# Kernel tuning notes

Measured on AMD Instinct MI355X. Metric: run time of the kernel, lower is better.

Reference implementation:

```python
import jax, jax.numpy as jnp
import numpy as np

DIM = 256
HEADS = 4
HEAD_DIM = DIM // HEADS          # 64
KEY_DIM = HEAD_DIM // 2          # 32 (attn_ratio=0.5)
HIDDEN = DIM + 2 * KEY_DIM * HEADS  # 512
B, H, W = 2, 64, 64
EPS = 1e-5


def _conv2d(x, w, groups=1, pad=0):
    return jax.lax.conv_general_dilated(
        x, w, window_strides=(1, 1), padding=[(pad, pad), (pad, pad)],
        dimension_numbers=('NCHW', 'OIHW', 'NCHW'), feature_group_count=groups)


def _bn(x, g, b, m, v):
    scale = g / jnp.sqrt(v + EPS)
    return x * scale[None, :, None, None] + (b - m * scale)[None, :, None, None]


def setup_inputs() -> dict:
    key = jax.random.key(0)
    ks = jax.random.split(key, 16)
    d = {
        'x': jax.random.normal(ks[0], (B, DIM, H, W), jnp.float32),
        'qkv_w': jax.random.normal(ks[1], (HIDDEN, DIM, 1, 1), jnp.float32) * 0.05,
        'qkv_g': jax.random.uniform(ks[2], (HIDDEN,), jnp.float32, 0.5, 1.5),
        'qkv_b': jax.random.normal(ks[3], (HIDDEN,), jnp.float32) * 0.1,
        'qkv_m': jax.random.normal(ks[4], (HIDDEN,), jnp.float32) * 0.1,
        'qkv_v': jax.random.uniform(ks[5], (HIDDEN,), jnp.float32, 0.5, 1.5),
        'proj_w': jax.random.normal(ks[6], (DIM, DIM, 1, 1), jnp.float32) * 0.05,
        'proj_g': jax.random.uniform(ks[7], (DIM,), jnp.float32, 0.5, 1.5),
        'proj_b': jax.random.normal(ks[8], (DIM,), jnp.float32) * 0.1,
        'proj_m': jax.random.normal(ks[9], (DIM,), jnp.float32) * 0.1,
        'proj_v': jax.random.uniform(ks[10], (DIM,), jnp.float32, 0.5, 1.5),
        'pe_w': jax.random.normal(ks[11], (DIM, 1, 3, 3), jnp.float32) * 0.1,
        'pe_g': jax.random.uniform(ks[12], (DIM,), jnp.float32, 0.5, 1.5),
        'pe_b': jax.random.normal(ks[13], (DIM,), jnp.float32) * 0.1,
        'pe_m': jax.random.normal(ks[14], (DIM,), jnp.float32) * 0.1,
        'pe_v': jax.random.uniform(ks[15], (DIM,), jnp.float32, 0.5, 1.5),
    }
    return d


def reference(x, qkv_w, qkv_g, qkv_b, qkv_m, qkv_v,
              proj_w, proj_g, proj_b, proj_m, proj_v,
              pe_w, pe_g, pe_b, pe_m, pe_v):
    b, c, h, w = x.shape
    n = h * w
    scale = KEY_DIM ** -0.5

    qkv = _bn(_conv2d(x, qkv_w), qkv_g, qkv_b, qkv_m, qkv_v)  # [b, hidden, h, w]
    qkv = qkv.reshape(b, HEADS, 2 * KEY_DIM + HEAD_DIM, n)
    q = qkv[:, :, :KEY_DIM]                       # [b, heads, key_dim, n]
    k = qkv[:, :, KEY_DIM:2 * KEY_DIM]            # [b, heads, key_dim, n]
    v = qkv[:, :, 2 * KEY_DIM:]                   # [b, heads, head_dim, n]

    # attn[b,h,i,j] = sum_d q[b,h,d,i] * k[b,h,d,j] * scale; softmax over j
    attn = jnp.einsum('bhdi,bhdj->bhij', q, k) * scale
    attn = jax.nn.softmax(attn, axis=-1)

    # y = v @ attn^T : out[b,h,d,i] = sum_j v[b,h,d,j] * attn[b,h,i,j]
    y = jnp.einsum('bhdj,bhij->bhdi', v, attn).reshape(b, c, h, w)

    pe = _bn(_conv2d(v.reshape(b, c, h, w), pe_w, groups=c, pad=1),
             pe_g, pe_b, pe_m, pe_v)
    y = y + pe
    return _bn(_conv2d(y, proj_w), proj_g, proj_b, proj_m, proj_v)
```

## Files before the change

kernel.cpp:

```cpp
#include <hip/hip_runtime.h>
#include <hip/hip_bf16.h>

#define NSP 4096
#define BEPS 1e-5f
#define JSPLIT 4
#define JCHUNK (NSP / JSPLIT)

using short8  = __attribute__((ext_vector_type(8))) short;
using f32x4   = __attribute__((ext_vector_type(4))) float;

#define SCALE_LOG2E 0.25500526940103816f

__device__ __forceinline__ float b2f(unsigned short u) {
  return __uint_as_float(((unsigned)u) << 16);
}
__device__ __forceinline__ float b2f_lo(unsigned w) {
  return __uint_as_float(w << 16);
}
__device__ __forceinline__ float b2f_hi(unsigned w) {
  return __uint_as_float(w & 0xffff0000u);
}
__device__ __forceinline__ unsigned short f2b(float x) {
  unsigned u = __float_as_uint(x);
  u += 0x7fffu + ((u >> 16) & 1u);
  return (unsigned short)(u >> 16);
}
__device__ __forceinline__ unsigned pk_bf16(float a, float b) {
  return ((unsigned)f2b(b) << 16) | (unsigned)f2b(a);
}
__device__ __forceinline__ unsigned pk2u(float a, float b) {
  __hip_bfloat162 h = __float22bfloat162_rn(float2{a, b});
  unsigned r;
  __builtin_memcpy(&r, &h, sizeof(r));
  return r;
}

__global__ __launch_bounds__(256) void cast_w_kernel(
    const float* __restrict__ qkv_w, const float* __restrict__ proj_w,
    unsigned short* __restrict__ wqb, unsigned short* __restrict__ wpb)
{
  const int i = blockIdx.x * 256 + threadIdx.x;
  if (i < 131072)       wqb[i] = f2b(qkv_w[i]);
  else                  wpb[i - 131072] = f2b(proj_w[i - 131072]);
}

__global__ __launch_bounds__(256) void transpose_x_kernel(
    const float* __restrict__ x, unsigned short* __restrict__ xT)
{
  const int n0 = blockIdx.x * 64, c0 = blockIdx.y * 64, b = blockIdx.z;
  __shared__ __align__(16) unsigned short tx[64][72];
  const int t = threadIdx.x;
  const int row = t >> 2;
  const int seg = t & 3;
  {
    const float* xp = x + ((size_t)(b * 256 + c0 + row)) * NSP + n0 + seg * 16;
    #pragma unroll
    for (int q4 = 0; q4 < 4; ++q4) {
      const float4 a = *reinterpret_cast<const float4*>(xp + q4 * 4);
      tx[seg * 16 + q4 * 4 + 0][row] = f2b(a.x);
      tx[seg * 16 + q4 * 4 + 1][row] = f2b(a.y);
      tx[seg * 16 + q4 * 4 + 2][row] = f2b(a.z);
      tx[seg * 16 + q4 * 4 + 3][row] = f2b(a.w);
    }
  }
  __syncthreads();
  const int nrow = t >> 2, ch = t & 3;
  unsigned short* op = xT + ((size_t)(b * NSP + n0 + nrow)) * 256 + c0 + ch * 16;
  *reinterpret_cast<float4*>(op)     = *reinterpret_cast<const float4*>(&tx[nrow][ch * 16]);
  *reinterpret_cast<float4*>(op + 8) = *reinterpret_cast<const float4*>(&tx[nrow][ch * 16 + 8]);
}

__global__ __launch_bounds__(256) void qkv_gemm_kernel(
    const unsigned short* __restrict__ xT, const unsigned short* __restrict__ wqb,
    const float* __restrict__ gg, const float* __restrict__ bb,
    const float* __restrict__ mm, const float* __restrict__ vv,
    unsigned short* __restrict__ qb, unsigned short* __restrict__ kb,
    unsigned short* __restrict__ vb)
{
  const int n0 = blockIdx.x * 128;
  const int cotile = blockIdx.y;
  const int b = blockIdx.z;
  const int co0 = cotile * 64;
  const int t = threadIdx.x;
  __shared__ __align__(16) unsigned short wt[64][136];
  __shared__ __align__(16) unsigned short xt[128][136];
  const int lane = t & 63, wave = t >> 6;
  const int m16 = lane & 15, quad = lane >> 4;

  f32x4 acc[8] = {};
  for (int kc = 0; kc < 2; ++kc) {
    if (kc) __syncthreads();
    {
      const unsigned short* wp = wqb + (size_t)(co0 + (t >> 2)) * 256 + kc * 128 + (t & 3) * 32;
      #pragma unroll
      for (int u = 0; u < 4; ++u)
        *reinterpret_cast<float4*>(&wt[t >> 2][(t & 3) * 32 + u * 8]) =
            *reinterpret_cast<const float4*>(wp + u * 8);
      const unsigned short* xp = xT + ((size_t)(b * NSP + n0 + (t >> 1))) * 256 + kc * 128 + (t & 1) * 64;
      #pragma unroll
      for (int u = 0; u < 8; ++u)
        *reinterpret_cast<float4*>(&xt[t >> 1][(t & 1) * 64 + u * 8]) =
            *reinterpret_cast<const float4*>(xp + u * 8);
    }
    __syncthreads();
    if ((cotile & 1) == 0) {
      #pragma unroll
      for (int ks = 0; ks < 4; ++ks) {
        const short8 af = *reinterpret_cast<const short8*>(&wt[wave * 16 + m16][ks * 32 + quad * 8]);
        #pragma unroll
        for (int nt = 0; nt < 8; ++nt) {
          const short8 bf = *reinterpret_cast<const short8*>(&xt[nt * 16 + m16][ks * 32 + quad * 8]);
          acc[nt] = __builtin_amdgcn_mfma_f32_16x16x32_bf16(af, bf, acc[nt], 0, 0, 0);
        }
      }
    } else {
      #pragma unroll
      for (int ks = 0; ks < 4; ++ks) {
        const short8 bf = *reinterpret_cast<const short8*>(&wt[wave * 16 + m16][ks * 32 + quad * 8]);
        #pragma unroll
        for (int nt = 0; nt < 8; ++nt) {
          const short8 af = *reinterpret_cast<const short8*>(&xt[nt * 16 + m16][ks * 32 + quad * 8]);
          acc[nt] = __builtin_amdgcn_mfma_f32_16x16x32_bf16(af, bf, acc[nt], 0, 0, 0);
        }
      }
    }
  }

  const int head = cotile >> 1;
  const int bh = b * 4 + head;
  if ((cotile & 1) == 0) {
    const int coh = wave * 16 + quad * 4;
    const bool isq = (coh < 32);
    const float fold = isq ? SCALE_LOG2E : 1.0f;
    float sc[4], bi[4];
    #pragma unroll
    for (int r = 0; r < 4; ++r) {
      const int c = co0 + coh + r;
      sc[r] = gg[c] * rsqrtf(vv[c] + BEPS) * fold;
      bi[r] = (bb[c] - mm[c] * gg[c] * rsqrtf(vv[c] + BEPS)) * fold;
    }
    unsigned short* dst = isq ? qb : kb;
    const int d0 = coh & 31;
    #pragma unroll
    for (int nt = 0; nt < 8; ++nt) {
      const int i = n0 + nt * 16 + m16;
      uint2 pk2;
      pk2.x = pk_bf16(acc[nt][0] * sc[0] + bi[0], acc[nt][1] * sc[1] + bi[1]);
      pk2.y = pk_bf16(acc[nt][2] * sc[2] + bi[2], acc[nt][3] * sc[3] + bi[3]);
      *reinterpret_cast<uint2*>(dst + ((size_t)bh * NSP + i) * 32 + d0) = pk2;
    }
  } else {
    const int c = co0 + wave * 16 + m16;
    const float sc = gg[c] * rsqrtf(vv[c] + BEPS);
    const float bi = bb[c] - mm[c] * sc;
    const int d = wave * 16 + m16;
    #pragma unroll
    for (int nt = 0; nt < 8; ++nt) {
      const int j = n0 + nt * 16 + quad * 4;
      uint2 pk2;
      pk2.x = pk_bf16(acc[nt][0] * sc + bi, acc[nt][1] * sc + bi);
      pk2.y = pk_bf16(acc[nt][2] * sc + bi, acc[nt][3] * sc + bi);
      *reinterpret_cast<uint2*>(vb + ((size_t)(bh * 64 + d)) * NSP + j) = pk2;
    }
  }
}

__global__ __launch_bounds__(256, 4) void attn_kernel(
    const unsigned short* __restrict__ qb, const unsigned short* __restrict__ kb,
    const unsigned short* __restrict__ vb,
    unsigned short* __restrict__ Opart, float* __restrict__ lpart)
{
  const int i0    = blockIdx.x * 128;
  const int bh    = blockIdx.y;
  const int split = blockIdx.z;
  const int jbase = split * JCHUNK;
  const int t  = threadIdx.x;
  const int lane = t & 63, wave = t >> 6;
  const int m16 = lane & 15, quad = lane >> 4;
  __shared__ __align__(16) short smem[16384];
  short (*qs)[40] = (short(*)[40])smem;
  short (*ps)[72] = (short(*)[72])smem;
  short (*ks)[40] = (short(*)[40])(smem + 9216);
  short (*vs)[72] = (short(*)[72])(smem + 9216 + 2560);

  {
    const unsigned short* qp = qb + ((size_t)bh * NSP + i0) * 32;
    const int r = t >> 1, h = t & 1;
    *reinterpret_cast<float4*>(&qs[r][h * 16]) =
        *reinterpret_cast<const float4*>(qp + r * 32 + h * 16);
    *reinterpret_cast<float4*>(&qs[r][h * 16 + 8]) =
        *reinterpret_cast<const float4*>(qp + r * 32 + h * 16 + 8);
  }
  __syncthreads();
  short8 qfrag[2];
  qfrag[0] = *reinterpret_cast<const short8*>(&qs[wave * 32 + m16][quad * 8]);
  qfrag[1] = *reinterpret_cast<const short8*>(&qs[wave * 32 + 16 + m16][quad * 8]);

  float rsum[2] = {0.f, 0.f};
  f32x4 oacc[2][4] = {};

  const int srow = t >> 2, schunk = t & 3;
  const unsigned short* kbase = kb + (size_t)bh * NSP * 32;
  const unsigned short* vbase = vb + (size_t)bh * 64 * NSP;

  float4 kreg, vreg0, vreg1;
  kreg  = *reinterpret_cast<const float4*>(kbase + (size_t)(jbase + srow) * 32 + schunk * 8);
  vreg0 = *reinterpret_cast<const float4*>(vbase + (size_t)srow * NSP + jbase + schunk * 16);
  vreg1 = *reinterpret_cast<const float4*>(vbase + (size_t)srow * NSP + jbase + schunk * 16 + 8);
  *reinterpret_cast<float4*>(&ks[srow][schunk * 8]) = kreg;
  *reinterpret_cast<float4*>(&vs[srow][schunk * 16]) = vreg0;
  *reinterpret_cast<float4*>(&vs[srow][schunk * 16 + 8]) = vreg1;
  __syncthreads();

  for (int jt0 = 0; jt0 < JCHUNK; jt0 += 64) {
    const bool more = (jt0 + 64) < JCHUNK;
    if (more) {
      const int jn = jbase + jt0 + 64;
      kreg  = *reinterpret_cast<const float4*>(kbase + (size_t)(jn + srow) * 32 + schunk * 8);
      vreg0 = *reinterpret_cast<const float4*>(vbase + (size_t)srow * NSP + jn + schunk * 16);
      vreg1 = *reinterpret_cast<const float4*>(vbase + (size_t)srow * NSP + jn + schunk * 16 + 8);
    }

    short8 kf[4];
    #pragma unroll
    for (int jt = 0; jt < 4; ++jt)
      kf[jt] = *reinterpret_cast<const short8*>(&ks[jt * 16 + m16][quad * 8]);

    #pragma unroll
    for (int it = 0; it < 2; ++it) {
      f32x4 sacc[4];
      #pragma unroll
      for (int jt = 0; jt < 4; ++jt)
        sacc[jt] = __builtin_amdgcn_mfma_f32_16x16x32_bf16(kf[jt], qfrag[it],
                                                           (f32x4){0.f,0.f,0.f,0.f}, 0, 0, 0);
      const int irow = wave * 32 + it * 16 + m16;
      #pragma unroll
      for (int jt = 0; jt < 4; ++jt) {
        float p0 = __builtin_amdgcn_exp2f(sacc[jt][0]);
        float p1 = __builtin_amdgcn_exp2f(sacc[jt][1]);
        float p2 = __builtin_amdgcn_exp2f(sacc[jt][2]);
        float p3 = __builtin_amdgcn_exp2f(sacc[jt][3]);
        rsum[it] += (p0 + p1) + (p2 + p3);
        uint2 pk2;
        pk2.x = pk2u(p0, p1);
        pk2.y = pk2u(p2, p3);
        *reinterpret_cast<uint2*>(&ps[irow][jt * 16 + quad * 4]) = pk2;
      }
    }

    short8 pa[2][2];
    #pragma unroll
    for (int it = 0; it < 2; ++it) {
      pa[it][0] = *reinterpret_cast<const short8*>(&ps[wave * 32 + it * 16 + m16][quad * 8]);
      pa[it][1] = *reinterpret_cast<const short8*>(&ps[wave * 32 + it * 16 + m16][32 + quad * 8]);
    }
    #pragma unroll
    for (int dt = 0; dt < 4; ++dt) {
      const short8 v0 = *reinterpret_cast<const short8*>(&vs[dt * 16 + m16][quad * 8]);
      const short8 v1 = *reinterpret_cast<const short8*>(&vs[dt * 16 + m16][32 + quad * 8]);
      #pragma unroll
      for (int it = 0; it < 2; ++it) {
        oacc[it][dt] = __builtin_amdgcn_mfma_f32_16x16x32_bf16(pa[it][0], v0, oacc[it][dt], 0, 0, 0);
        oacc[it][dt] = __builtin_amdgcn_mfma_f32_16x16x32_bf16(pa[it][1], v1, oacc[it][dt], 0, 0, 0);
      }
    }

    if (more) {
      __syncthreads();
      *reinterpret_cast<float4*>(&ks[srow][schunk * 8]) = kreg;
      *reinterpret_cast<float4*>(&vs[srow][schunk * 16]) = vreg0;
      *reinterpret_cast<float4*>(&vs[srow][schunk * 16 + 8]) = vreg1;
      __syncthreads();
    }
  }

  #pragma unroll
  for (int it = 0; it < 2; ++it) {
    float rs = rsum[it];
    rs += __shfl_xor(rs, 16);
    rs += __shfl_xor(rs, 32);
    if (quad == 0)
      lpart[((size_t)split * 8 + bh) * NSP + i0 + wave * 32 + it * 16 + m16] = rs;
  }

  #pragma unroll
  for (int it = 0; it < 2; ++it)
    #pragma unroll
    for (int dt = 0; dt < 4; ++dt) {
      const int d = dt * 16 + m16;
      uint2 pk2;
      pk2.x = pk2u(oacc[it][dt][0], oacc[it][dt][1]);
      pk2.y = pk2u(oacc[it][dt][2], oacc[it][dt][3]);
      *reinterpret_cast<uint2*>(Opart +
          (((size_t)split * 8 + bh) * 64 + d) * NSP + i0 + wave * 32 + it * 16 + quad * 4) = pk2;
    }
}

__global__ __launch_bounds__(256) void fuse_kernel(
    const unsigned short* __restrict__ Opart, const float* __restrict__ lpart,
    const unsigned short* __restrict__ vb,
    const float* __restrict__ pw, const float* __restrict__ pg,
    const float* __restrict__ pb, const float* __restrict__ pm,
    const float* __restrict__ pv,
    unsigned short* __restrict__ yT)
{
  const int py = blockIdx.x;
  const int bh = blockIdx.y;
  const int b = bh >> 2, h = bh & 3;
  const int t = threadIdx.x;
  const int d = t >> 2, seg = t & 3;
  __shared__ float lsum[64];
  __shared__ __align__(16) unsigned short yt[64][72];

  if (t < 64) {
    float ls = 0.f;
    #pragma unroll
    for (int s = 0; s < JSPLIT; ++s)
      ls += lpart[((size_t)s * 8 + bh) * NSP + py * 64 + t];
    lsum[t] = ls;
  }
  __syncthreads();

  const int c = h * 64 + d;
  const int i0 = py * 64 + seg * 16;
  float os[16] = {};
  #pragma unroll
  for (int s = 0; s < JSPLIT; ++s) {
    const uint4* op = reinterpret_cast<const uint4*>(
        Opart + (((size_t)s * 8 + bh) * 64 + d) * NSP + i0);
    const uint4 a = op[0], e = op[1];
    os[0]  += b2f_lo(a.x); os[1]  += b2f_hi(a.x);
    os[2]  += b2f_lo(a.y); os[3]  += b2f_hi(a.y);
    os[4]  += b2f_lo(a.z); os[5]  += b2f_hi(a.z);
    os[6]  += b2f_lo(a.w); os[7]  += b2f_hi(a.w);
    os[8]  += b2f_lo(e.x); os[9]  += b2f_hi(e.x);
    os[10] += b2f_lo(e.y); os[11] += b2f_hi(e.y);
    os[12] += b2f_lo(e.z); os[13] += b2f_hi(e.z);
    os[14] += b2f_lo(e.w); os[15] += b2f_hi(e.w);
  }

  float w9[9];
  #pragma unroll
  for (int i = 0; i < 9; ++i) w9[i] = pw[c * 9 + i];
  const float sc = pg[c] * rsqrtf(pv[c] + BEPS);
  const float bi = pb[c] - pm[c] * sc;
  const unsigned short* vrow = vb + ((size_t)(bh * 64 + d)) * NSP;

  float conv[16] = {};
  #pragma unroll
  for (int dy = -1; dy <= 1; ++dy) {
    const int yy = py + dy;
    if (yy < 0 || yy > 63) continue;
    const unsigned short* vr = vrow + yy * 64 + seg * 16;
    float vals[18];
    const uint4 m0 = *reinterpret_cast<const uint4*>(vr);
    const uint4 m1 = *reinterpret_cast<const uint4*>(vr + 8);
    vals[1]  = b2f_lo(m0.x); vals[2]  = b2f_hi(m0.x);
    vals[3]  = b2f_lo(m0.y); vals[4]  = b2f_hi(m0.y);
    vals[5]  = b2f_lo(m0.z); vals[6]  = b2f_hi(m0.z);
    vals[7]  = b2f_lo(m0.w); vals[8]  = b2f_hi(m0.w);
    vals[9]  = b2f_lo(m1.x); vals[10] = b2f_hi(m1.x);
    vals[11] = b2f_lo(m1.y); vals[12] = b2f_hi(m1.y);
    vals[13] = b2f_lo(m1.z); vals[14] = b2f_hi(m1.z);
    vals[15] = b2f_lo(m1.w); vals[16] = b2f_hi(m1.w);
    vals[0]  = (seg > 0) ? b2f_hi(*reinterpret_cast<const unsigned*>(vr - 2)) : 0.f;
    vals[17] = (seg < 3) ? b2f_lo(*reinterpret_cast<const unsigned*>(vr + 16)) : 0.f;
    const float wr0 = w9[(dy + 1) * 3 + 0], wr1 = w9[(dy + 1) * 3 + 1], wr2 = w9[(dy + 1) * 3 + 2];
    #pragma unroll
    for (int u = 0; u < 16; ++u)
      conv[u] += vals[u] * wr0 + vals[u + 1] * wr1 + vals[u + 2] * wr2;
  }

  #pragma unroll
  for (int u = 0; u < 16; ++u) {
    const float yv = os[u] / lsum[seg * 16 + u] + conv[u] * sc + bi;
    yt[seg * 16 + u][d] = f2b(yv);
  }
  __syncthreads();

  const int prow = t >> 2, ch = t & 3;
  unsigned short* op = yT + ((size_t)(b * NSP + py * 64 + prow)) * 256 + h * 64 + ch * 16;
  *reinterpret_cast<float4*>(op)     = *reinterpret_cast<const float4*>(&yt[prow][ch * 16]);
  *reinterpret_cast<float4*>(op + 8) = *reinterpret_cast<const float4*>(&yt[prow][ch * 16 + 8]);
}

__global__ __launch_bounds__(256) void proj_gemm_kernel(
    const unsigned short* __restrict__ yT, const unsigned short* __restrict__ wpb,
    const float* __restrict__ gg, const float* __restrict__ bb,
    const float* __restrict__ mm, const float* __restrict__ vv,
    float* __restrict__ out)
{
  const int n0 = blockIdx.x * 128;
  const int co0 = blockIdx.y * 64;
  const int b = blockIdx.z;
  const int t = threadIdx.x;
  __shared__ __align__(16) unsigned short wt[64][136];
  __shared__ __align__(16) unsigned short yt[128][136];
  const int lane = t & 63, wave = t >> 6;
  const int m16 = lane & 15, quad = lane >> 4;

  f32x4 acc[8] = {};
  for (int kc = 0; kc < 2; ++kc) {
    if (kc) __syncthreads();
    {
      const unsigned short* wp = wpb + (size_t)(co0 + (t >> 2)) * 256 + kc * 128 + (t & 3) * 32;
      #pragma unroll
      for (int u = 0; u < 4; ++u)
        *reinterpret_cast<float4*>(&wt[t >> 2][(t & 3) * 32 + u * 8]) =
            *reinterpret_cast<const float4*>(wp + u * 8);
      const unsigned short* yp = yT + ((size_t)(b * NSP + n0 + (t >> 1))) * 256 + kc * 128 + (t & 1) * 64;
      #pragma unroll
      for (int u = 0; u < 8; ++u)
        *reinterpret_cast<float4*>(&yt[t >> 1][(t & 1) * 64 + u * 8]) =
            *reinterpret_cast<const float4*>(yp + u * 8);
    }
    __syncthreads();
    #pragma unroll
    for (int ks = 0; ks < 4; ++ks) {
      const short8 bf = *reinterpret_cast<const short8*>(&wt[wave * 16 + m16][ks * 32 + quad * 8]);
      #pragma unroll
      for (int nt = 0; nt < 8; ++nt) {
        const short8 af = *reinterpret_cast<const short8*>(&yt[nt * 16 + m16][ks * 32 + quad * 8]);
        acc[nt] = __builtin_amdgcn_mfma_f32_16x16x32_bf16(af, bf, acc[nt], 0, 0, 0);
      }
    }
  }

  const int c = co0 + wave * 16 + m16;
  const float sc = gg[c] * rsqrtf(vv[c] + BEPS);
  const float bi = bb[c] - mm[c] * sc;
  #pragma unroll
  for (int nt = 0; nt < 8; ++nt) {
    const int n = n0 + nt * 16 + quad * 4;
    float4 ov;
    ov.x = acc[nt][0] * sc + bi; ov.y = acc[nt][1] * sc + bi;
    ov.z = acc[nt][2] * sc + bi; ov.w = acc[nt][3] * sc + bi;
    *reinterpret_cast<float4*>(out + ((size_t)(b * 256 + c)) * NSP + n) = ov;
  }
}

extern "C" void kernel_launch(void* const* d_in, const int* in_sizes, int n_in,
                              void* d_out, int out_size, void* d_ws, size_t ws_size,
                              hipStream_t stream)
{
  const float* x      = (const float*)d_in[0];
  const float* qkv_w  = (const float*)d_in[1];
  const float* qkv_g  = (const float*)d_in[2];
  const float* qkv_b  = (const float*)d_in[3];
  const float* qkv_m  = (const float*)d_in[4];
  const float* qkv_v  = (const float*)d_in[5];
  const float* proj_w = (const float*)d_in[6];
  const float* proj_g = (const float*)d_in[7];
  const float* proj_b = (const float*)d_in[8];
  const float* proj_m = (const float*)d_in[9];
  const float* proj_v = (const float*)d_in[10];
  const float* pe_w   = (const float*)d_in[11];
  const float* pe_g   = (const float*)d_in[12];
  const float* pe_b   = (const float*)d_in[13];
  const float* pe_m   = (const float*)d_in[14];
  const float* pe_v   = (const float*)d_in[15];
  float* out = (float*)d_out;

  unsigned short* qb = (unsigned short*)d_ws;
  unsigned short* kb = qb + (size_t)8 * NSP * 32;
  unsigned short* vb = kb + (size_t)8 * NSP * 32;
  unsigned short* Opart = vb + (size_t)8 * 64 * NSP;
  float* lpart = (float*)(Opart + (size_t)JSPLIT * 8 * 64 * NSP);
  unsigned short* xT = (unsigned short*)(lpart + (size_t)JSPLIT * 8 * NSP);
  unsigned short* yT = xT + (size_t)2 * NSP * 256;
  unsigned short* wqb = yT + (size_t)2 * NSP * 256;
  unsigned short* wpb = wqb + (size_t)512 * 256;

  cast_w_kernel<<<dim3(768), 256, 0, stream>>>(qkv_w, proj_w, wqb, wpb);
  transpose_x_kernel<<<dim3(64, 4, 2), 256, 0, stream>>>(x, xT);
  qkv_gemm_kernel<<<dim3(32, 8, 2), 256, 0, stream>>>(xT, wqb, qkv_g, qkv_b, qkv_m, qkv_v,
                                                      qb, kb, vb);
  attn_kernel<<<dim3(32, 8, JSPLIT), 256, 0, stream>>>(qb, kb, vb, Opart, lpart);
  fuse_kernel<<<dim3(64, 8), 256, 0, stream>>>(Opart, lpart, vb,
                                               pe_w, pe_g, pe_b, pe_m, pe_v, yT);
  proj_gemm_kernel<<<dim3(32, 4, 2), 256, 0, stream>>>(yT, wpb, proj_g, proj_b, proj_m, proj_v,
                                                       out);
}
```

Baseline: 157.2 us.

## Keep softmax probabilities in registers and feed PV MFMA directly

```diff
diff --git a/kernel.cpp b/kernel.cpp
--- a/kernel.cpp
+++ b/kernel.cpp
@@ -7,6 +7,7 @@
 #define JCHUNK (NSP / JSPLIT)
 
 using short8  = __attribute__((ext_vector_type(8))) short;
+using short4v = __attribute__((ext_vector_type(4))) short;
 using f32x4   = __attribute__((ext_vector_type(4))) float;
 
 #define SCALE_LOG2E 0.25500526940103816f
@@ -33,6 +34,14 @@
   unsigned r;
   __builtin_memcpy(&r, &h, sizeof(r));
   return r;
+}
+__device__ __forceinline__ short4v pk4(float a, float b, float c, float d) {
+  uint2 u;
+  u.x = pk2u(a, b);
+  u.y = pk2u(c, d);
+  short4v v;
+  __builtin_memcpy(&v, &u, 8);
+  return v;
 }
 
 __global__ __launch_bounds__(256) void cast_w_kernel(
@@ -177,11 +186,9 @@
   const int t  = threadIdx.x;
   const int lane = t & 63, wave = t >> 6;
   const int m16 = lane & 15, quad = lane >> 4;
-  __shared__ __align__(16) short smem[16384];
-  short (*qs)[40] = (short(*)[40])smem;
-  short (*ps)[72] = (short(*)[72])smem;
-  short (*ks)[40] = (short(*)[40])(smem + 9216);
-  short (*vs)[72] = (short(*)[72])(smem + 9216 + 2560);
+  __shared__ __align__(16) short qs[128][40];
+  __shared__ __align__(16) short ks[64][40];
+  __shared__ __align__(16) short vs[64][72];
 
   {
     const unsigned short* qp = qb + ((size_t)bh * NSP + i0) * 32;
@@ -226,6 +233,7 @@
     for (int jt = 0; jt < 4; ++jt)
       kf[jt] = *reinterpret_cast<const short8*>(&ks[jt * 16 + m16][quad * 8]);
 
+    short4v pa[2][4];
     #pragma unroll
     for (int it = 0; it < 2; ++it) {
       f32x4 sacc[4];
@@ -233,7 +241,6 @@
       for (int jt = 0; jt < 4; ++jt)
         sacc[jt] = __builtin_amdgcn_mfma_f32_16x16x32_bf16(kf[jt], qfrag[it],
                                                            (f32x4){0.f,0.f,0.f,0.f}, 0, 0, 0);
-      const int irow = wave * 32 + it * 16 + m16;
       #pragma unroll
       for (int jt = 0; jt < 4; ++jt) {
         float p0 = __builtin_amdgcn_exp2f(sacc[jt][0]);
@@ -241,27 +248,20 @@
         float p2 = __builtin_amdgcn_exp2f(sacc[jt][2]);
         float p3 = __builtin_amdgcn_exp2f(sacc[jt][3]);
         rsum[it] += (p0 + p1) + (p2 + p3);
-        uint2 pk2;
-        pk2.x = pk2u(p0, p1);
-        pk2.y = pk2u(p2, p3);
-        *reinterpret_cast<uint2*>(&ps[irow][jt * 16 + quad * 4]) = pk2;
+        pa[it][jt] = pk4(p0, p1, p2, p3);
       }
     }
 
-    short8 pa[2][2];
-    #pragma unroll
-    for (int it = 0; it < 2; ++it) {
-      pa[it][0] = *reinterpret_cast<const short8*>(&ps[wave * 32 + it * 16 + m16][quad * 8]);
-      pa[it][1] = *reinterpret_cast<const short8*>(&ps[wave * 32 + it * 16 + m16][32 + quad * 8]);
-    }
     #pragma unroll
     for (int dt = 0; dt < 4; ++dt) {
-      const short8 v0 = *reinterpret_cast<const short8*>(&vs[dt * 16 + m16][quad * 8]);
-      const short8 v1 = *reinterpret_cast<const short8*>(&vs[dt * 16 + m16][32 + quad * 8]);
-      #pragma unroll
-      for (int it = 0; it < 2; ++it) {
-        oacc[it][dt] = __builtin_amdgcn_mfma_f32_16x16x32_bf16(pa[it][0], v0, oacc[it][dt], 0, 0, 0);
-        oacc[it][dt] = __builtin_amdgcn_mfma_f32_16x16x32_bf16(pa[it][1], v1, oacc[it][dt], 0, 0, 0);
+      #pragma unroll
+      for (int jt = 0; jt < 4; ++jt) {
+        const short4v vf = *reinterpret_cast<const short4v*>(
+            &vs[dt * 16 + m16][jt * 16 + quad * 4]);
+        #pragma unroll
+        for (int it = 0; it < 2; ++it)
+          oacc[it][dt] = __builtin_amdgcn_mfma_f32_16x16x16bf16_1k(pa[it][jt], vf,
+                                                                  oacc[it][dt], 0, 0, 0);
       }
     }
 
```

After: 160.3 us. Within noise of the previous version (+2.0%).
